# Kernel tuning notes

Hardware: AMD Instinct MI355X
Metric: run time of the kernel (lower is better)

## Reference

```python
import jax, jax.numpy as jnp
import numpy as np

TAU = 0.3
NEG_SLOPE = 0.2
COS_EPS = 1e-8


def _masked_softmax(logits, mask, axis):
    # mask: bool, True = participates. Rows with no True entries yield zeros.
    neg = jnp.finfo(logits.dtype).min
    x = jnp.where(mask, logits, neg)
    x = x - jnp.max(x, axis=axis, keepdims=True)
    e = jnp.exp(x) * mask
    return e / jnp.maximum(jnp.sum(e, axis=axis, keepdims=True), 1e-16)


def _gat_layer(h, adj, W, a_src, a_dst, w_edge, a_edge, b):
    # Dense masked GATConv (heads=1). adj[b,i,j]=True means edge src j -> dst i.
    g = jnp.einsum('bld,dc->blc', h, W)            # projected features
    al_s = jnp.einsum('blc,c->bl', g, a_src)        # per-node src score
    al_d = jnp.einsum('blc,c->bl', g, a_dst)        # per-node dst score
    # edge_attr is constant 1.0 for every thresholded edge, so the edge term
    # lin_edge(1.0) . att_edge collapses to a scalar.
    ae = jnp.dot(w_edge, a_edge)
    logits = jax.nn.leaky_relu(al_d[:, :, None] + al_s[:, None, :] + ae, NEG_SLOPE)
    attn = _masked_softmax(logits, adj, axis=-1)    # softmax over incoming edges per dst
    out = jnp.einsum('bij,bjc->bic', attn, g) + b
    return jax.nn.relu(out)


def setup_inputs() -> dict:
    key = jax.random.key(0)
    B, L, D, H = 16, 1024, 768, 128
    ks = jax.random.split(key, 20)
    inp = {}
    inp['hidden'] = jax.random.normal(ks[0], (B, L, D), jnp.float32)
    inp['attention_mask'] = jax.random.randint(ks[1], (B, L), 0, 2, jnp.int32)

    def lin(k, i, o):
        return jax.random.normal(k, (i, o), jnp.float32) * (1.0 / np.sqrt(i))

    dims = [D, H]
    for l in range(2):
        i = dims[l]
        inp[f'W{l}'] = lin(ks[2 + 6 * l], i, H)
        inp[f'att_src{l}'] = jax.random.normal(ks[3 + 6 * l], (H,), jnp.float32) * 0.1
        inp[f'att_dst{l}'] = jax.random.normal(ks[4 + 6 * l], (H,), jnp.float32) * 0.1
        inp[f'w_edge{l}'] = jax.random.normal(ks[5 + 6 * l], (H,), jnp.float32) * 0.1
        inp[f'att_edge{l}'] = jax.random.normal(ks[6 + 6 * l], (H,), jnp.float32) * 0.1
        inp[f'bias{l}'] = jnp.zeros((H,), jnp.float32)
    out_dim = D + 2 * H            # jk_mode='cat' -> 1024
    hid = max(128, out_dim // 2)   # 512
    inp['S1_W'] = lin(ks[14], out_dim, hid)
    inp['S1_b'] = jnp.zeros((hid,), jnp.float32)
    inp['S2_W'] = lin(ks[15], hid, 1)
    inp['S2_b'] = jnp.zeros((1,), jnp.float32)
    return inp


def reference(hidden, attention_mask,
              W0, att_src0, att_dst0, w_edge0, att_edge0, bias0,
              W1, att_src1, att_dst1, w_edge1, att_edge1, bias1,
              S1_W, S1_b, S2_W, S2_b):
    valid = attention_mask.astype(bool)                         # (B,L)
    # per-batch pairwise cosine similarity graph, thresholded at TAU
    nrm = jnp.linalg.norm(hidden, axis=-1, keepdims=True)
    hn = hidden / jnp.maximum(nrm, COS_EPS)
    sim = jnp.einsum('bld,bmd->blm', hn, hn)                    # (B,L,L)
    adj = (sim > TAU) & valid[:, :, None] & valid[:, None, :]   # bool mask; diag (self loops) kept, sim=1>tau

    h1 = _gat_layer(hidden, adj, W0, att_src0, att_dst0, w_edge0, att_edge0, bias0)
    h2 = _gat_layer(h1, adj, W1, att_src1, att_dst1, w_edge1, att_edge1, bias1)
    h_all = jnp.concatenate([hidden, h1, h2], axis=-1)          # jk 'cat': (B,L,D+2H)

    scores = (jnp.tanh(h_all @ S1_W + S1_b) @ S2_W + S2_b)[..., 0]  # (B,L)
    weights = _masked_softmax(scores, valid, axis=-1)           # segment softmax per batch element
    pooled = jnp.einsum('bl,bld->bd', weights, h_all)           # segment scatter_add pooling
    return pooled
```

## Files before the change

### kernel.cpp

```cpp
#include <hip/hip_runtime.h>

typedef __attribute__((ext_vector_type(8))) short short8;
typedef __attribute__((ext_vector_type(4))) short s4v;
typedef __attribute__((ext_vector_type(4))) float f32x4;
typedef unsigned short u16;
typedef unsigned int u32;
typedef unsigned long long u64;

#define TAU_F 0.3f

__device__ __forceinline__ u16 f2bf(float f){
  u32 u = __float_as_uint(f);
  u32 r = u + 0x7FFFu + ((u >> 16) & 1u);
  return (u16)(r >> 16);
}
__device__ __forceinline__ float bf2f(u16 v){
  return __uint_as_float(((u32)v) << 16);
}
__device__ __forceinline__ float tanh_fast(float x){
  const float e = __expf(2.f * x);
  return 1.f - 2.f / (e + 1.f);
}

typedef __attribute__((address_space(1))) const u32 glb_u32;
typedef __attribute__((address_space(3))) u32 lds_u32;
__device__ __forceinline__ void async_lds16(const void* g, void* l){
  __builtin_amdgcn_global_load_lds((glb_u32*)g, (lds_u32*)l, 16, 0, 0);
}

__global__ __launch_bounds__(1024)
void pre_kernel(float* __restrict__ out, float* __restrict__ scores,
                const float* __restrict__ W0, u16* __restrict__ w0t,
                const float* __restrict__ W1, u16* __restrict__ w1t,
                const float* __restrict__ S1W, u16* __restrict__ s1t,
                const float* __restrict__ wed0, const float* __restrict__ aed0,
                const float* __restrict__ wed1, const float* __restrict__ aed1,
                float* __restrict__ aeb,
                const float* __restrict__ asrc0, const float* __restrict__ adst0,
                const float* __restrict__ asrc1, const float* __restrict__ adst1,
                float* __restrict__ u0, float* __restrict__ v0,
                float* __restrict__ u1, float* __restrict__ v1,
                const int* __restrict__ mask, int* __restrict__ cnt, int* __restrict__ idxb)
{
  __shared__ float lds[64*65];
  const int blk = blockIdx.x, t = threadIdx.x;

  auto tr_tile = [&](const float* in, u16* o, int K, int N, int kt, int ntile) {
    const int r = t >> 4, c0 = (t & 15) * 4;
    const int k0 = kt*64, n0 = ntile*64;
    const float4 v = *(const float4*)&in[(long)(k0 + r)*N + n0 + c0];
    lds[r*65 + c0 + 0] = v.x; lds[r*65 + c0 + 1] = v.y;
    lds[r*65 + c0 + 2] = v.z; lds[r*65 + c0 + 3] = v.w;
    __syncthreads();
    const u64 pk = (u64)f2bf(lds[(c0+0)*65 + r])
                 | ((u64)f2bf(lds[(c0+1)*65 + r]) << 16)
                 | ((u64)f2bf(lds[(c0+2)*65 + r]) << 32)
                 | ((u64)f2bf(lds[(c0+3)*65 + r]) << 48);
    *(u64*)&o[(long)(n0 + r)*K + k0 + c0] = pk;
  };

  if (blk < 16)  { out[blk*1024 + t] = 0.f; return; }
  if (blk < 32)  { scores[(blk-16)*1024 + t] = 0.f; return; }
  if (blk < 56)  { const int id = blk-32;  tr_tile(W0,  w0t, 768, 128, id >> 1, id & 1); return; }
  if (blk < 60)  { const int id = blk-56;  tr_tile(W1,  w1t, 128, 128, id >> 1, id & 1); return; }
  if (blk < 188) { const int id = blk-60;  tr_tile(S1W, s1t, 1024, 512, id >> 3, id & 7); return; }
  if (blk == 188) {
    if (t < 128) { lds[t] = wed0[t]*aed0[t]; lds[128+t] = wed1[t]*aed1[t]; }
    __syncthreads();
    for (int o = 64; o > 0; o >>= 1) { if (t < o) { lds[t] += lds[t+o]; lds[128+t] += lds[128+t+o]; } __syncthreads(); }
    if (t == 0) { aeb[0] = lds[0]; aeb[1] = lds[128]; }
    return;
  }
  if (blk == 189) {
    if (t < 768) {
      float su = 0.f, sv = 0.f;
      for (int c = 0; c < 128; c++) { const float w = W0[t*128 + c]; su += w*asrc0[c]; sv += w*adst0[c]; }
      u0[t] = su; v0[t] = sv;
    }
    return;
  }
  if (blk == 190) {
    if (t < 128) {
      float su = 0.f, sv = 0.f;
      for (int k = 0; k < 128; k++) { const float w = W1[k*128 + t]; su += w*asrc1[k]; sv += w*adst1[k]; }
      u1[t] = su; v1[t] = sv;
    }
    return;
  }
  {
    int* wtot = (int*)lds;
    int* woff = (int*)lds + 16;
    const int b = blk - 191;
    const int w = t >> 6, lane = t & 63;
    const int m = mask[(b << 10) + t];
    const u64 bal = __ballot(m != 0);
    const int pos = __popcll(bal & ((1ull << lane) - 1ull));
    if (lane == 0) wtot[w] = __popcll(bal);
    __syncthreads();
    if (t == 0) { int a = 0; for (int i = 0; i < 16; i++) { woff[i] = a; a += wtot[i]; } cnt[b] = a; }
    __syncthreads();
    if (m) idxb[(b << 10) + woff[w] + pos] = t;
  }
}

__global__ __launch_bounds__(256)
void hn_kernel(const float* __restrict__ hidden, const int* __restrict__ cnt,
               const int* __restrict__ idx,
               const float* __restrict__ u0, const float* __restrict__ v0,
               const float* __restrict__ aeb,
               u16* __restrict__ hallc, float* __restrict__ rnp,
               float* __restrict__ als, float* __restrict__ ald)
{
  const int gr = blockIdx.x * 4 + (threadIdx.x >> 6);
  const int b = gr >> 10, c = gr & 1023;
  const int lane = threadIdx.x & 63;
  if (c >= cnt[b]) return;
  const int l = idx[gr];
  const float* h = hidden + (long)((b << 10) + l) * 768;
  float x[12]; float ss = 0.f, sa = 0.f, sd = 0.f;
#pragma unroll
  for (int k = 0; k < 12; k++) {
    x[k] = h[k*64 + lane];
    ss += x[k]*x[k];
    sa += x[k]*u0[k*64 + lane];
    sd += x[k]*v0[k*64 + lane];
  }
#pragma unroll
  for (int o = 32; o > 0; o >>= 1) {
    ss += __shfl_xor(ss, o, 64);
    sa += __shfl_xor(sa, o, 64);
    sd += __shfl_xor(sd, o, 64);
  }
  const float inv = 1.f / fmaxf(sqrtf(ss), 1e-8f);
  if (lane == 0) { als[gr] = sa; ald[gr] = sd + aeb[0]; rnp[gr] = inv; }
#pragma unroll
  for (int k = 0; k < 12; k++)
    hallc[(long)gr*1024 + k*64 + lane] = f2bf(x[k]);
}

__global__ __launch_bounds__(256)
void mega_kernel(const u16* __restrict__ hallc, const u16* __restrict__ w0t,
                 const u16* __restrict__ s1t, const float* __restrict__ rn,
                 unsigned char* __restrict__ adjp, u16* __restrict__ gtp,
                 u16* __restrict__ partial, const int* __restrict__ cnt)
{
  __shared__ u16 lA[2][64*64];
  __shared__ u16 lB[2][64*64];
  const int t = threadIdx.x, w = t >> 6, lane = t & 63;
  const int bid = blockIdx.x;
  int mode, bz = 0, i0, n0, lda, ldb, ti = 0, tj = 0, cb = 0;
  const u16 *Ab, *Bb;
  if (bid < 2176) {
    mode = 0;
    const int xcd = bid & 7, s = bid >> 3;
    const int hi = (s >= 136) ? 1 : 0;
    bz = xcd*2 + hi;
    int rem = s - hi*136, width = 16;
    while (rem >= width) { rem -= width; ti++; width--; }
    tj = ti + rem;
    i0 = ti*64; n0 = tj*64;
    cb = cnt[bz];
    if (i0 >= cb || n0 >= cb) return;
    Ab = hallc + (((long)bz << 10) << 10);
    Bb = Ab; lda = 1024; ldb = 1024;
  } else if (bid < 2688) {
    mode = 1;
    const int id = bid - 2176;
    i0 = (((id & 7) << 5) + ((id >> 3) & 31)) * 64;
    n0 = (id >> 8) * 64;
    if ((i0 & 1023) >= cnt[i0 >> 10]) return;
    Ab = hallc; lda = 1024; Bb = w0t; ldb = 768;
  } else {
    mode = 2;
    const int id = bid - 2688;
    i0 = (((id & 7) << 5) + ((id >> 3) & 31)) * 64;
    n0 = (id >> 8) * 64;
    if ((i0 & 1023) >= cnt[i0 >> 10]) return;
    Ab = hallc; lda = 1024; Bb = s1t; ldb = 1024;
  }
  const int wr = w >> 1, wc = w & 1;
  const int srow = t >> 3, scg = t & 7;
  const int sc0 = ((scg ^ (srow & 7)) << 3);
  const long arow0 = (long)(i0 + srow) * lda, arow1 = (long)(i0 + srow + 32) * lda;
  const long brow0 = (long)(n0 + srow) * ldb, brow1 = (long)(n0 + srow + 32) * ldb;
  const int rA = lane & 15, kg = lane >> 4;
  const int sw = rA & 7;
  const int off0 = ((kg ^ sw) << 3);
  const int off1 = (((4 + kg) ^ sw) << 3);
  const int rowA0 = (wr*32 + rA) * 64, rowA1 = (wr*32 + 16 + rA) * 64;
  const int rowB0 = (wc*32 + rA) * 64, rowB1 = (wc*32 + 16 + rA) * 64;
  f32x4 acc[2][2] = {};

  auto stage = [&](int buf, int kt) {
    async_lds16(Ab + arow0 + kt + sc0, &lA[buf][t*8]);
    async_lds16(Ab + arow1 + kt + sc0, &lA[buf][2048 + t*8]);
    async_lds16(Bb + brow0 + kt + sc0, &lB[buf][t*8]);
    async_lds16(Bb + brow1 + kt + sc0, &lB[buf][2048 + t*8]);
  };
  auto compute = [&](int buf) {
    short8 a00 = *(const short8*)&lA[buf][rowA0 + off0];
    short8 a01 = *(const short8*)&lA[buf][rowA0 + off1];
    short8 a10 = *(const short8*)&lA[buf][rowA1 + off0];
    short8 a11 = *(const short8*)&lA[buf][rowA1 + off1];
    short8 b00 = *(const short8*)&lB[buf][rowB0 + off0];
    short8 b01 = *(const short8*)&lB[buf][rowB0 + off1];
    short8 b10 = *(const short8*)&lB[buf][rowB1 + off0];
    short8 b11 = *(const short8*)&lB[buf][rowB1 + off1];
    acc[0][0] = __builtin_amdgcn_mfma_f32_16x16x32_bf16(a00, b00, acc[0][0], 0, 0, 0);
    acc[0][1] = __builtin_amdgcn_mfma_f32_16x16x32_bf16(a00, b10, acc[0][1], 0, 0, 0);
    acc[1][0] = __builtin_amdgcn_mfma_f32_16x16x32_bf16(a10, b00, acc[1][0], 0, 0, 0);
    acc[1][1] = __builtin_amdgcn_mfma_f32_16x16x32_bf16(a10, b10, acc[1][1], 0, 0, 0);
    acc[0][0] = __builtin_amdgcn_mfma_f32_16x16x32_bf16(a01, b01, acc[0][0], 0, 0, 0);
    acc[0][1] = __builtin_amdgcn_mfma_f32_16x16x32_bf16(a01, b11, acc[0][1], 0, 0, 0);
    acc[1][0] = __builtin_amdgcn_mfma_f32_16x16x32_bf16(a11, b01, acc[1][0], 0, 0, 0);
    acc[1][1] = __builtin_amdgcn_mfma_f32_16x16x32_bf16(a11, b11, acc[1][1], 0, 0, 0);
  };

  stage(0, 0);
  __syncthreads();
  int cur = 0;
  for (int kt = 1; kt < 12; kt++) {
    stage(cur ^ 1, kt << 6);
    compute(cur);
    __syncthreads();
    cur ^= 1;
  }
  compute(cur);

#pragma unroll
  for (int m = 0; m < 2; m++) {
    const int gi0 = i0 + wr*32 + m*16 + kg*4;
#pragma unroll
    for (int n = 0; n < 2; n++) {
      const int gj = n0 + wc*32 + n*16 + rA;
#pragma unroll
      for (int r = 0; r < 4; r++) {
        const int gi = gi0 + r;
        const float c = acc[m][n][r];
        if (mode == 0) {
          if (gi < cb && gj < cb) {
            const float sim = c * rn[(bz << 10) + gi] * rn[(bz << 10) + gj];
            const unsigned char e = (sim > TAU_F) ? 1 : 0;
            adjp[((long)bz << 20) + ((long)gi << 10) + gj] = e;
            if (ti != tj) adjp[((long)bz << 20) + ((long)gj << 10) + gi] = e;
          }
        } else if (mode == 1) {
          const int b = gi >> 10, l = gi & 1023;
          gtp[(((long)(b*128 + gj)) << 10) + l] = f2bf(c);
        } else {
          partial[(long)gi * 512 + gj] = f2bf(c);
        }
      }
    }
  }
}

__global__ __launch_bounds__(256)
void scorer_fin(const u16* __restrict__ hallc, const u16* __restrict__ s1t,
                const u16* __restrict__ partial, const int* __restrict__ cnt,
                const float* __restrict__ s1b, const float* __restrict__ s2w,
                float* __restrict__ scoresp)
{
  __shared__ u16 lA[2][64*64];
  __shared__ u16 lB[2][64*64];
  __shared__ float sgrid[64];
  const int t = threadIdx.x, w = t >> 6, lane = t & 63;
  const int id = blockIdx.x;
  const int i0 = (((id & 7) << 5) + ((id >> 3) & 31)) * 64;
  const int n0 = (id >> 8) * 64;
  if ((i0 & 1023) >= cnt[i0 >> 10]) return;
  if (t < 64) sgrid[t] = 0.f;
  const int wr = w >> 1, wc = w & 1;
  const int srow = t >> 3, scg = t & 7;
  const int sc0 = ((scg ^ (srow & 7)) << 3);
  const long arow0 = (long)(i0 + srow) * 1024 + 768, arow1 = (long)(i0 + srow + 32) * 1024 + 768;
  const long brow0 = (long)(n0 + srow) * 1024 + 768, brow1 = (long)(n0 + srow + 32) * 1024 + 768;
  const int rA = lane & 15, kg = lane >> 4;
  const int sw = rA & 7;
  const int off0 = ((kg ^ sw) << 3);
  const int off1 = (((4 + kg) ^ sw) << 3);
  const int rowA0 = (wr*32 + rA) * 64, rowA1 = (wr*32 + 16 + rA) * 64;
  const int rowB0 = (wc*32 + rA) * 64, rowB1 = (wc*32 + 16 + rA) * 64;
  f32x4 acc[2][2] = {};

  auto stage = [&](int buf, int kt) {
    async_lds16(hallc + arow0 + kt + sc0, &lA[buf][t*8]);
    async_lds16(hallc + arow1 + kt + sc0, &lA[buf][2048 + t*8]);
    async_lds16(s1t + brow0 + kt + sc0, &lB[buf][t*8]);
    async_lds16(s1t + brow1 + kt + sc0, &lB[buf][2048 + t*8]);
  };
  auto compute = [&](int buf) {
    short8 a00 = *(const short8*)&lA[buf][rowA0 + off0];
    short8 a01 = *(const short8*)&lA[buf][rowA0 + off1];
    short8 a10 = *(const short8*)&lA[buf][rowA1 + off0];
    short8 a11 = *(const short8*)&lA[buf][rowA1 + off1];
    short8 b00 = *(const short8*)&lB[buf][rowB0 + off0];
    short8 b01 = *(const short8*)&lB[buf][rowB0 + off1];
    short8 b10 = *(const short8*)&lB[buf][rowB1 + off0];
    short8 b11 = *(const short8*)&lB[buf][rowB1 + off1];
    acc[0][0] = __builtin_amdgcn_mfma_f32_16x16x32_bf16(a00, b00, acc[0][0], 0, 0, 0);
    acc[0][1] = __builtin_amdgcn_mfma_f32_16x16x32_bf16(a00, b10, acc[0][1], 0, 0, 0);
    acc[1][0] = __builtin_amdgcn_mfma_f32_16x16x32_bf16(a10, b00, acc[1][0], 0, 0, 0);
    acc[1][1] = __builtin_amdgcn_mfma_f32_16x16x32_bf16(a10, b10, acc[1][1], 0, 0, 0);
    acc[0][0] = __builtin_amdgcn_mfma_f32_16x16x32_bf16(a01, b01, acc[0][0], 0, 0, 0);
    acc[0][1] = __builtin_amdgcn_mfma_f32_16x16x32_bf16(a01, b11, acc[0][1], 0, 0, 0);
    acc[1][0] = __builtin_amdgcn_mfma_f32_16x16x32_bf16(a11, b01, acc[1][0], 0, 0, 0);
    acc[1][1] = __builtin_amdgcn_mfma_f32_16x16x32_bf16(a11, b11, acc[1][1], 0, 0, 0);
  };

  stage(0, 0);
  __syncthreads();
  int cur = 0;
  for (int kt = 1; kt < 4; kt++) {
    stage(cur ^ 1, kt << 6);
    compute(cur);
    __syncthreads();
    cur ^= 1;
  }
  compute(cur);

#pragma unroll
  for (int m = 0; m < 2; m++)
#pragma unroll
    for (int r = 0; r < 4; r++) {
      const int gi = i0 + wr*32 + m*16 + kg*4 + r;
      float contrib = 0.f;
#pragma unroll
      for (int n = 0; n < 2; n++) {
        const int gj = n0 + wc*32 + n*16 + rA;
        const float p = acc[m][n][r] + bf2f(partial[(long)gi*512 + gj]) + s1b[gj];
        contrib += tanh_fast(p) * s2w[gj];
      }
#pragma unroll
      for (int off = 1; off < 16; off <<= 1) contrib += __shfl_xor(contrib, off, 64);
      if (rA == 0) atomicAdd(&sgrid[wr*32 + m*16 + kg*4 + r], contrib);
    }
  __syncthreads();
  if (t < 64) {
    const int gi = i0 + t;
    if ((gi & 1023) < cnt[gi >> 10]) atomicAdd(&scoresp[gi], sgrid[t]);
  }
}

template<int FUSE>
__global__ __launch_bounds__(256)
void gat_attn(const unsigned char* __restrict__ adj,
              const float* __restrict__ ald, const float* __restrict__ als,
              const u16* __restrict__ gT, const float* __restrict__ bias,
              const int* __restrict__ cnt,
              u16* __restrict__ hall, int hall_off,
              const float* __restrict__ u1, const float* __restrict__ v1,
              const float* __restrict__ aeb1,
              float* __restrict__ als_o, float* __restrict__ ald_o,
              const u16* __restrict__ w1t, u16* __restrict__ gt2)
{
  __shared__ float red[4][16][132];
  __shared__ float ssumw[4][16];
  __shared__ float alds[FUSE ? 16 : 1][17], aldd[FUSE ? 16 : 1][17];
  __shared__ u16 h1s[FUSE ? 16 : 1][136];
  const int t = threadIdx.x, w = t >> 6, lane = t & 63;
  const int o = blockIdx.x;
  const int xcd = o & 7, s = o >> 3;
  const int bz = xcd*2 + (s >> 6);
  const int i0 = (s & 63) * 16;
  const int cb = cnt[bz];
  if (i0 >= cb) return;
  const int rr = lane & 15, kg = lane >> 4;
  const int r0 = i0 + rr;
  const bool rvalid = r0 < cb;
  const float ald0 = ald[(bz << 10) + r0];
  const unsigned char* arow = adj + ((long)bz << 20) + ((long)r0 << 10);
  const float* als_b = als + (bz << 10);
  const u16* gTb = gT + ((long)bz << 17);
  float s0 = 0.f;
  f32x4 acc[8] = {};
  const int jbase = w * 256 + kg * 8;

  u64 aw[8];
#pragma unroll
  for (int it = 0; it < 8; it++) {
    const int jl = jbase + it*32;
    u64 a = 0;
    if (rvalid && jl < cb) {
      a = *(const u64*)(arow + jl);
      const int rem = cb - jl;
      if (rem < 8) a &= (1ull << (rem * 8)) - 1ull;
    }
    aw[it] = a;
  }

#pragma unroll
  for (int it = 0; it < 8; it++) {
    const u64 a0 = aw[it];
    if (__any(a0 != 0ull)) {
      const int jl = jbase + it*32;
      const float4 f0 = *(const float4*)(als_b + jl);
      const float4 f1 = *(const float4*)(als_b + jl + 4);
      const float sv[8] = {f0.x, f0.y, f0.z, f0.w, f1.x, f1.y, f1.z, f1.w};
      short8 pa;
#pragma unroll
      for (int e = 0; e < 8; e++) {
        float x = ald0 + sv[e];
        x = x > 0.f ? x : 0.2f * x;
        const float p = ((a0 >> (8*e)) & 255ull) ? __expf(x) : 0.f;
        s0 += p;
        pa[e] = (short)f2bf(p);
      }
#pragma unroll
      for (int nf = 0; nf < 8; nf++) {
        const short8 b = *(const short8*)&gTb[(long)(nf*16 + rr) * 1024 + jl];
        acc[nf] = __builtin_amdgcn_mfma_f32_16x16x32_bf16(pa, b, acc[nf], 0, 0, 0);
      }
    }
  }

  s0 += __shfl_xor(s0, 16, 64);
  s0 += __shfl_xor(s0, 32, 64);
  if (lane < 16) ssumw[w][lane] = s0;
#pragma unroll
  for (int nf = 0; nf < 8; nf++)
#pragma unroll
    for (int rg = 0; rg < 4; rg++)
      red[w][kg*4 + rg][nf*16 + rr] = acc[nf][rg];
  __syncthreads();

  const int r = t >> 4, c0 = (t & 15) * 8;
  const float sm = ssumw[0][r] + ssumw[1][r] + ssumw[2][r] + ssumw[3][r];
  const float inv = sm > 0.f ? 1.f / sm : 0.f;
  const long gi = ((long)bz << 10) + i0 + r;
  u16* orow = hall + gi * 1024 + hall_off;
  short8 hv;
  float pa_s = 0.f, pa_d = 0.f;
#pragma unroll
  for (int q = 0; q < 8; q++) {
    const int c = c0 + q;
    float v = (red[0][r][c] + red[1][r][c] + red[2][r][c] + red[3][r][c]) * inv + bias[c];
    v = v > 0.f ? v : 0.f;
    hv[q] = (short)f2bf(v);
    if (FUSE) { pa_s += v * u1[c]; pa_d += v * v1[c]; }
  }
  *(short8*)&orow[c0] = hv;
  if (FUSE) {
    *(short8*)&h1s[r][c0] = hv;
    alds[r][t & 15] = pa_s;
    aldd[r][t & 15] = pa_d;
    __syncthreads();
    if (t < 16) {
      float s2 = 0.f, d2 = 0.f;
#pragma unroll
      for (int j = 0; j < 16; j++) { s2 += alds[t][j]; d2 += aldd[t][j]; }
      als_o[(bz << 10) + i0 + t] = s2;
      ald_o[(bz << 10) + i0 + t] = d2 + aeb1[0];
    }
    f32x4 pacc[2] = {};
    short8 paf[4];
#pragma unroll
    for (int ks = 0; ks < 4; ks++)
      paf[ks] = *(const short8*)&h1s[lane & 15][ks*32 + kg*8];
#pragma unroll
    for (int n = 0; n < 2; n++) {
      const int col = w*32 + n*16 + (lane & 15);
#pragma unroll
      for (int ks = 0; ks < 4; ks++) {
        const short8 pb = *(const short8*)&w1t[col*128 + ks*32 + kg*8];
        pacc[n] = __builtin_amdgcn_mfma_f32_16x16x32_bf16(paf[ks], pb, pacc[n], 0, 0, 0);
      }
    }
#pragma unroll
    for (int n = 0; n < 2; n++) {
      const int gj = w*32 + n*16 + (lane & 15);
#pragma unroll
      for (int rg = 0; rg < 4; rg++)
        gt2[(((long)(bz*128 + gj)) << 10) + i0 + kg*4 + rg] = f2bf(pacc[n][rg]);
    }
  }
}

__global__ __launch_bounds__(256)
void pooled_kernel(const u16* __restrict__ hallc, const float* __restrict__ scores,
                   const int* __restrict__ cnt, float* __restrict__ out)
{
  __shared__ float tot[4];
  const int b = blockIdx.y, l0 = blockIdx.x * 64, t = threadIdx.x;
  const int cb = cnt[b];
  if (l0 >= cb) return;
  float part = 0.f;
#pragma unroll
  for (int q = 0; q < 4; q++) {
    const int l = q*256 + t;
    if (l < cb) part += __expf(scores[(b << 10) + l]);
  }
#pragma unroll
  for (int o = 32; o > 0; o >>= 1) part += __shfl_xor(part, o, 64);
  if ((t & 63) == 0) tot[t >> 6] = part;
  __syncthreads();
  const float inv = 1.f / fmaxf(tot[0] + tot[1] + tot[2] + tot[3], 1e-16f);

  const int lim = min(64, cb - l0);
  float a0 = 0.f, a1 = 0.f, a2 = 0.f, a3 = 0.f;
  for (int l = 0; l < lim; l++) {
    const int gl = (b << 10) + l0 + l;
    const float wv = __expf(scores[gl]) * inv;
    const s4v v = *(const s4v*)&hallc[(long)gl*1024 + t*4];
    a0 += wv * bf2f((u16)v[0]);
    a1 += wv * bf2f((u16)v[1]);
    a2 += wv * bf2f((u16)v[2]);
    a3 += wv * bf2f((u16)v[3]);
  }
  atomicAdd(&out[(b<<10) + t*4 + 0], a0);
  atomicAdd(&out[(b<<10) + t*4 + 1], a1);
  atomicAdd(&out[(b<<10) + t*4 + 2], a2);
  atomicAdd(&out[(b<<10) + t*4 + 3], a3);
}

extern "C" void kernel_launch(void* const* d_in, const int* in_sizes, int n_in,
                              void* d_out, int out_size, void* d_ws, size_t ws_size,
                              hipStream_t stream)
{
  const float* hidden = (const float*)d_in[0];
  const int*   mask   = (const int*)d_in[1];
  const float* W0     = (const float*)d_in[2];
  const float* asrc0  = (const float*)d_in[3];
  const float* adst0  = (const float*)d_in[4];
  const float* wed0   = (const float*)d_in[5];
  const float* aed0   = (const float*)d_in[6];
  const float* bias0  = (const float*)d_in[7];
  const float* W1     = (const float*)d_in[8];
  const float* asrc1  = (const float*)d_in[9];
  const float* adst1  = (const float*)d_in[10];
  const float* wed1   = (const float*)d_in[11];
  const float* aed1   = (const float*)d_in[12];
  const float* bias1  = (const float*)d_in[13];
  const float* S1W    = (const float*)d_in[14];
  const float* S1b    = (const float*)d_in[15];
  const float* S2W    = (const float*)d_in[16];
  float* out = (float*)d_out;

  char* ws = (char*)d_ws;
  u16* hallc   = (u16*)(ws + 0);
  u16* partial = (u16*)(ws + 33554432);
  u16* gt2     = (u16*)(ws + 50331648);
  unsigned char* adj = (unsigned char*)(ws + 58720256);
  u16* gt   = (u16*)(ws + 75497472);
  u16* w0t  = (u16*)(ws + 79691776);
  u16* w1t  = (u16*)(ws + 79888384);
  u16* s1t  = (u16*)(ws + 79921152);
  float* ald = (float*)(ws + 80969728);
  float* als = (float*)(ws + 81035264);
  float* scores = (float*)(ws + 81100800);
  float* als1   = (float*)(ws + 81166336);
  float* ald1   = (float*)(ws + 81231872);
  float* aeb    = (float*)(ws + 81297408);
  int*   cnt    = (int*)(ws + 81297920);
  int*   idxb   = (int*)(ws + 81298432);
  float* u0     = (float*)(ws + 81363968);
  float* v0     = (float*)(ws + 81367040);
  float* u1     = (float*)(ws + 81370112);
  float* v1     = (float*)(ws + 81370624);
  float* rn     = (float*)(ws + 81371136);

  pre_kernel<<<207, 1024, 0, stream>>>(out, scores, W0, w0t, W1, w1t, S1W, s1t,
      wed0, aed0, wed1, aed1, aeb, asrc0, adst0, asrc1, adst1,
      u0, v0, u1, v1, mask, cnt, idxb);

  hn_kernel<<<4096, 256, 0, stream>>>(hidden, cnt, idxb, u0, v0, aeb, hallc, rn, als, ald);

  mega_kernel<<<4736, 256, 0, stream>>>(hallc, w0t, s1t, rn, adj, gt, partial, cnt);

  gat_attn<1><<<1024, 256, 0, stream>>>(adj, ald, als, gt, bias0, cnt, hallc, 768,
        u1, v1, aeb + 1, als1, ald1, w1t, gt2);

  gat_attn<0><<<1024, 256, 0, stream>>>(adj, ald1, als1, gt2, bias1, cnt, hallc, 896,
        nullptr, nullptr, nullptr, nullptr, nullptr, nullptr, nullptr);

  scorer_fin<<<2048, 256, 0, stream>>>(hallc, s1t, partial, cnt, S1b, S2W, scores);

  pooled_kernel<<<dim3(16,16), 256, 0, stream>>>(hallc, scores, cnt, out);
}
```

Measured before the change: 115.1 us.

## Enlarge mega_kernel GEMM tiles to 128x64 with per-wave 32x64 outputs

Switches the fused GEMM kernel from 64x64 to 128x64 output tiles. Each wave now computes a 32x64 slab with 8 MFMA accumulators, so B fragments are reused across more MFMAs and fewer blocks are launched. The triangular tiling for the similarity GEMM is rewritten for 128-row tiles, and the mirrored adjacency write is now gated by gi<gj. The trade-off is more LDS and registers per block and fewer blocks, which may reduce occupancy and load balance across batches with varying valid counts.

```diff
diff --git a/kernel.cpp b/kernel.cpp
--- a/kernel.cpp
+++ b/kernel.cpp
@@ -144,76 +144,77 @@
                  unsigned char* __restrict__ adjp, u16* __restrict__ gtp,
                  u16* __restrict__ partial, const int* __restrict__ cnt)
 {
-  __shared__ u16 lA[2][64*64];
+  __shared__ u16 lA[2][128*64];
   __shared__ u16 lB[2][64*64];
   const int t = threadIdx.x, w = t >> 6, lane = t & 63;
   const int bid = blockIdx.x;
-  int mode, bz = 0, i0, n0, lda, ldb, ti = 0, tj = 0, cb = 0;
+  int mode, bz = 0, i0, n0, lda, ldb, cb = 0;
   const u16 *Ab, *Bb;
-  if (bid < 2176) {
+  if (bid < 1152) {
     mode = 0;
     const int xcd = bid & 7, s = bid >> 3;
-    const int hi = (s >= 136) ? 1 : 0;
+    const int hi = (s >= 72) ? 1 : 0;
     bz = xcd*2 + hi;
-    int rem = s - hi*136, width = 16;
-    while (rem >= width) { rem -= width; ti++; width--; }
-    tj = ti + rem;
-    i0 = ti*64; n0 = tj*64;
+    int rem = s - hi*72, width = 16, ti = 0;
+    while (rem >= width) { rem -= width; ti++; width -= 2; }
+    const int tj = 2*ti + rem;
+    i0 = ti*128; n0 = tj*64;
     cb = cnt[bz];
     if (i0 >= cb || n0 >= cb) return;
-    Ab = hallc + (((long)bz << 10) << 10);
+    Ab = hallc + ((long)bz << 20);
     Bb = Ab; lda = 1024; ldb = 1024;
-  } else if (bid < 2688) {
+  } else if (bid < 1408) {
     mode = 1;
-    const int id = bid - 2176;
-    i0 = (((id & 7) << 5) + ((id >> 3) & 31)) * 64;
-    n0 = (id >> 8) * 64;
+    const int id = bid - 1152;
+    const int y = (id & 7) + ((id >> 4) << 3);
+    i0 = y * 128; n0 = ((id >> 3) & 1) * 64;
     if ((i0 & 1023) >= cnt[i0 >> 10]) return;
     Ab = hallc; lda = 1024; Bb = w0t; ldb = 768;
   } else {
     mode = 2;
-    const int id = bid - 2688;
-    i0 = (((id & 7) << 5) + ((id >> 3) & 31)) * 64;
-    n0 = (id >> 8) * 64;
+    const int id = bid - 1408;
+    const int y = (id & 7) + ((id >> 6) << 3);
+    i0 = y * 128; n0 = ((id >> 3) & 7) * 64;
     if ((i0 & 1023) >= cnt[i0 >> 10]) return;
     Ab = hallc; lda = 1024; Bb = s1t; ldb = 1024;
   }
-  const int wr = w >> 1, wc = w & 1;
   const int srow = t >> 3, scg = t & 7;
   const int sc0 = ((scg ^ (srow & 7)) << 3);
-  const long arow0 = (long)(i0 + srow) * lda, arow1 = (long)(i0 + srow + 32) * lda;
-  const long brow0 = (long)(n0 + srow) * ldb, brow1 = (long)(n0 + srow + 32) * ldb;
   const int rA = lane & 15, kg = lane >> 4;
   const int sw = rA & 7;
   const int off0 = ((kg ^ sw) << 3);
   const int off1 = (((4 + kg) ^ sw) << 3);
-  const int rowA0 = (wr*32 + rA) * 64, rowA1 = (wr*32 + 16 + rA) * 64;
-  const int rowB0 = (wc*32 + rA) * 64, rowB1 = (wc*32 + 16 + rA) * 64;
-  f32x4 acc[2][2] = {};
+  f32x4 acc[2][4] = {};
 
   auto stage = [&](int buf, int kt) {
-    async_lds16(Ab + arow0 + kt + sc0, &lA[buf][t*8]);
-    async_lds16(Ab + arow1 + kt + sc0, &lA[buf][2048 + t*8]);
-    async_lds16(Bb + brow0 + kt + sc0, &lB[buf][t*8]);
-    async_lds16(Bb + brow1 + kt + sc0, &lB[buf][2048 + t*8]);
+#pragma unroll
+    for (int q = 0; q < 4; q++)
+      async_lds16(Ab + (long)(i0 + srow + q*32) * lda + kt + sc0, &lA[buf][q*2048 + t*8]);
+#pragma unroll
+    for (int q = 0; q < 2; q++)
+      async_lds16(Bb + (long)(n0 + srow + q*32) * ldb + kt + sc0, &lB[buf][q*2048 + t*8]);
   };
   auto compute = [&](int buf) {
-    short8 a00 = *(const short8*)&lA[buf][rowA0 + off0];
-    short8 a01 = *(const short8*)&lA[buf][rowA0 + off1];
-    short8 a10 = *(const short8*)&lA[buf][rowA1 + off0];
-    short8 a11 = *(const short8*)&lA[buf][rowA1 + off1];
-    short8 b00 = *(const short8*)&lB[buf][rowB0 + off0];
-    short8 b01 = *(const short8*)&lB[buf][rowB0 + off1];
-    short8 b10 = *(const short8*)&lB[buf][rowB1 + off0];
-    short8 b11 = *(const short8*)&lB[buf][rowB1 + off1];
-    acc[0][0] = __builtin_amdgcn_mfma_f32_16x16x32_bf16(a00, b00, acc[0][0], 0, 0, 0);
-    acc[0][1] = __builtin_amdgcn_mfma_f32_16x16x32_bf16(a00, b10, acc[0][1], 0, 0, 0);
-    acc[1][0] = __builtin_amdgcn_mfma_f32_16x16x32_bf16(a10, b00, acc[1][0], 0, 0, 0);
-    acc[1][1] = __builtin_amdgcn_mfma_f32_16x16x32_bf16(a10, b10, acc[1][1], 0, 0, 0);
-    acc[0][0] = __builtin_amdgcn_mfma_f32_16x16x32_bf16(a01, b01, acc[0][0], 0, 0, 0);
-    acc[0][1] = __builtin_amdgcn_mfma_f32_16x16x32_bf16(a01, b11, acc[0][1], 0, 0, 0);
-    acc[1][0] = __builtin_amdgcn_mfma_f32_16x16x32_bf16(a11, b01, acc[1][0], 0, 0, 0);
-    acc[1][1] = __builtin_amdgcn_mfma_f32_16x16x32_bf16(a11, b11, acc[1][1], 0, 0, 0);
+    short8 a[2][2], b[4][2];
+#pragma unroll
+    for (int m = 0; m < 2; m++) {
+      const int ra = (w*32 + m*16 + rA) * 64;
+      a[m][0] = *(const short8*)&lA[buf][ra + off0];
+      a[m][1] = *(const short8*)&lA[buf][ra + off1];
+    }
+#pragma unroll
+    for (int n = 0; n < 4; n++) {
+      const int rb = (n*16 + rA) * 64;
+      b[n][0] = *(const short8*)&lB[buf][rb + off0];
+      b[n][1] = *(const short8*)&lB[buf][rb + off1];
+    }
+#pragma unroll
+    for (int m = 0; m < 2; m++)
+#pragma unroll
+      for (int n = 0; n < 4; n++) {
+        acc[m][n] = __builtin_amdgcn_mfma_f32_16x16x32_bf16(a[m][0], b[n][0], acc[m][n], 0, 0, 0);
+        acc[m][n] = __builtin_amdgcn_mfma_f32_16x16x32_bf16(a[m][1], b[n][1], acc[m][n], 0, 0, 0);
+      }
   };
 
   stage(0, 0);
@@ -229,10 +230,10 @@
 
 #pragma unroll
   for (int m = 0; m < 2; m++) {
-    const int gi0 = i0 + wr*32 + m*16 + kg*4;
-#pragma unroll
-    for (int n = 0; n < 2; n++) {
-      const int gj = n0 + wc*32 + n*16 + rA;
+    const int gi0 = i0 + w*32 + m*16 + kg*4;
+#pragma unroll
+    for (int n = 0; n < 4; n++) {
+      const int gj = n0 + n*16 + rA;
 #pragma unroll
       for (int r = 0; r < 4; r++) {
         const int gi = gi0 + r;
@@ -242,7 +243,7 @@
             const float sim = c * rn[(bz << 10) + gi] * rn[(bz << 10) + gj];
             const unsigned char e = (sim > TAU_F) ? 1 : 0;
             adjp[((long)bz << 20) + ((long)gi << 10) + gj] = e;
-            if (ti != tj) adjp[((long)bz << 20) + ((long)gj << 10) + gi] = e;
+            if (gi < gj) adjp[((long)bz << 20) + ((long)gj << 10) + gi] = e;
           }
         } else if (mode == 1) {
           const int b = gi >> 10, l = gi & 1023;
@@ -565,7 +566,7 @@
 
   hn_kernel<<<4096, 256, 0, stream>>>(hidden, cnt, idxb, u0, v0, aeb, hallc, rn, als, ald);
 
-  mega_kernel<<<4736, 256, 0, stream>>>(hallc, w0t, s1t, rn, adj, gt, partial, cnt);
+  mega_kernel<<<2432, 256, 0, stream>>>(hallc, w0t, s1t, rn, adj, gt, partial, cnt);
 
   gat_attn<1><<<1024, 256, 0, stream>>>(adj, ald, als, gt, bias0, cnt, hallc, 768,
         u1, v1, aeb + 1, als1, ald1, w1t, gt2);
```

New measurement: 120.8 us. 5.0% more time.
